# Performance work log

Measured on AMD Instinct MI355X. Metric: run time of the kernel, lower is better.

Reference implementation:

```python
import jax, jax.numpy as jnp
import numpy as np
import math

_B, _L, _D, _H = 4, 2048, 512, 8
_DH = _D // _H


def setup_inputs() -> dict:
    key = jax.random.key(0)
    ks = jax.random.split(key, 16)
    w_scale = 1.0 / math.sqrt(_D)
    def lin(kw, kb):
        W = jax.random.uniform(kw, (_D, _D), jnp.float32, -w_scale, w_scale)
        b = jax.random.uniform(kb, (_D,), jnp.float32, -w_scale, w_scale)
        return W, b
    Wq_w, Wq_b = lin(ks[0], ks[1])
    Wk_w, Wk_b = lin(ks[2], ks[3])
    Wv_w, Wv_b = lin(ks[4], ks[5])
    fc_w, fc_b = lin(ks[6], ks[7])
    Q = jax.random.normal(ks[8], (_B, _L, _D), jnp.float32)
    K = jax.random.normal(ks[9], (_B, _L, _D), jnp.float32)
    V = jax.random.normal(ks[10], (_B, _L, _D), jnp.float32)
    # E = torch.rand(L, DH): uniform [0,1), non-trainable buffer
    E = jax.random.uniform(ks[11], (_L, _DH), jnp.float32)
    # causal mask: True (1) where attention is disallowed -> gets -1e9
    mask = jnp.triu(jnp.ones((_L, _L), dtype=bool), k=1)[None, None]  # (1,1,L,L)
    return {"Q": Q, "K": K, "V": V, "mask": mask,
            "Wq_w": Wq_w, "Wq_b": Wq_b, "Wk_w": Wk_w, "Wk_b": Wk_b,
            "Wv_w": Wv_w, "Wv_b": Wv_b, "fc_w": fc_w, "fc_b": fc_b,
            "E": E, "H": _H}


def reference(Q, K, V, mask, Wq_w, Wq_b, Wk_w, Wk_b, Wv_w, Wv_b, fc_w, fc_b, E, H):
    B, Lq, D = Q.shape
    DH = D // H

    def proj(x, W, b):  # torch Linear: x @ W.T + b, then split heads -> (B,H,L,DH)
        y = x @ W.T + b
        return y.reshape(B, -1, H, DH).transpose(0, 2, 1, 3)

    q = proj(Q, Wq_w, Wq_b)
    k = proj(K, Wk_w, Wk_b)
    v = proj(V, Wv_w, Wv_b)
    Lk = k.shape[2]

    # _get_left_embedding: last Lq rows of E
    Eu = E[max(0, E.shape[0] - Lq):, :]            # (e, DH), e == Lq here
    e = Eu.shape[0]

    QE = jnp.einsum('bhld,ed->bhle', q, Eu)        # (B,H,Lq,e)
    # _qe_masking: keep QE[..., i, j] where j >= e-1-i (upper anti-triangle)
    i = jnp.arange(Lq)[:, None]
    j = jnp.arange(e)[None, :]
    keep = (i + j >= e - 1).astype(QE.dtype)
    QE = QE * keep

    # _skewing: pad one zero column, reshape, drop first row
    padded = jnp.pad(QE, ((0, 0), (0, 0), (0, 0), (1, 0)))   # (B,H,Lq,e+1)
    Srel = padded.reshape(B, H, e + 1, Lq)[:, :, 1:, :]      # (B,H,e,Lq)
    if Lk < Lq:
        Srel = Srel[:, :, :, :Lk]

    logits = (jnp.einsum('bhld,bhmd->bhlm', q, k) + Srel) / math.sqrt(DH)
    logits = logits + mask.astype(jnp.float32) * (-1e9)
    AW = jax.nn.softmax(logits, axis=-1)
    out = jnp.einsum('bhlm,bhmd->bhld', AW, v)               # (B,H,Lq,DH)
    out = out.transpose(0, 2, 1, 3).reshape(B, -1, D)        # (B,Lq,D)
    return out @ fc_w.T + fc_b
```

## Files before the change

kernel.cpp:

```cpp
#include <hip/hip_runtime.h>
#include <stdint.h>

typedef __bf16 bf16;
typedef float f32x4 __attribute__((ext_vector_type(4)));
typedef bf16 bf16x8 __attribute__((ext_vector_type(8)));
typedef bf16 bf16x4 __attribute__((ext_vector_type(4)));

#define MFMA16(a, b, c) __builtin_amdgcn_mfma_f32_16x16x32_bf16((a), (b), (c), 0, 0, 0)
#define EXP2F(x) __builtin_amdgcn_exp2f(x)

__device__ __forceinline__ void gll16(const void* g, void* l) {
  __builtin_amdgcn_global_load_lds((const __attribute__((address_space(1))) void*)g,
                                   (__attribute__((address_space(3))) void*)l, 16, 0, 0);
}

__global__ __launch_bounds__(256) void convert_all(
    const float4* __restrict__ Q, const float4* __restrict__ K, const float4* __restrict__ V,
    const float4* __restrict__ Wq, const float4* __restrict__ Wk, const float4* __restrict__ Wv,
    const float4* __restrict__ fcw, const float4* __restrict__ E,
    bf16x4* __restrict__ Xq, bf16x4* __restrict__ Xk, bf16x4* __restrict__ Xv,
    bf16x4* __restrict__ Wqb, bf16x4* __restrict__ Wkb, bf16x4* __restrict__ Wvb,
    bf16x4* __restrict__ fcb, bf16x4* __restrict__ Eb) {
  int i = blockIdx.x * 256 + threadIdx.x;
  const float4* s;
  bf16x4* d;
  int off;
  if (i < 1048576) { s = Q; d = Xq; off = i; }
  else if (i < 2097152) { s = K; d = Xk; off = i - 1048576; }
  else if (i < 3145728) { s = V; d = Xv; off = i - 2097152; }
  else if (i < 3211264) { s = Wq; d = Wqb; off = i - 3145728; }
  else if (i < 3276800) { s = Wk; d = Wkb; off = i - 3211264; }
  else if (i < 3342336) { s = Wv; d = Wvb; off = i - 3276800; }
  else if (i < 3407872) { s = fcw; d = fcb; off = i - 3342336; }
  else { s = E; d = Eb; off = i - 3407872; }
  float4 v = s[off];
  bf16x4 o;
  o[0] = (bf16)v.x; o[1] = (bf16)v.y; o[2] = (bf16)v.z; o[3] = (bf16)v.w;
  d[off] = o;
}

__device__ __forceinline__ void gemm_core(const bf16* __restrict__ A, const bf16* __restrict__ Bt,
                                          bf16* ldsA, bf16* ldsB, int m0, int n0,
                                          f32x4 acc[4][4]) {
  const int t = threadIdx.x;
  const int lane = t & 63, w = t >> 6;
  const int l15 = lane & 15, quad = lane >> 4;
  const int wm = w >> 1, wn = w & 1;
#pragma unroll
  for (int i = 0; i < 4; i++)
#pragma unroll
    for (int j = 0; j < 4; j++) acc[i][j] = (f32x4){0.f, 0.f, 0.f, 0.f};

  const int ch0 = t, ch1 = t + 256;
  const int r0 = ch0 >> 2, c0 = (ch0 & 3) ^ (r0 & 3);
  const int r1 = ch1 >> 2, c1 = (ch1 & 3) ^ (r1 & 3);

  int aoff[4], boff[4];
#pragma unroll
  for (int mt = 0; mt < 4; mt++) {
    int m = wm * 64 + mt * 16 + l15;
    aoff[mt] = (m << 6) + ((quad ^ (l15 & 3)) << 4);
    int n = wn * 64 + mt * 16 + l15;
    boff[mt] = (n << 6) + ((quad ^ (l15 & 3)) << 4);
  }
  bf16* ldsA1 = ldsA + w * 512;
  bf16* ldsA2 = ldsA + 2048 + w * 512;
  bf16* ldsB1 = ldsB + w * 512;
  bf16* ldsB2 = ldsB + 2048 + w * 512;

  for (int kt = 0; kt < 512; kt += 32) {
    gll16(A + (size_t)(m0 + r0) * 512 + kt + c0 * 8, ldsA1);
    gll16(A + (size_t)(m0 + r1) * 512 + kt + c1 * 8, ldsA2);
    gll16(Bt + (size_t)(n0 + r0) * 512 + kt + c0 * 8, ldsB1);
    gll16(Bt + (size_t)(n0 + r1) * 512 + kt + c1 * 8, ldsB2);
    __syncthreads();
    bf16x8 af[4], bfr[4];
#pragma unroll
    for (int mt = 0; mt < 4; mt++) af[mt] = *(const bf16x8*)((const char*)ldsA + aoff[mt]);
#pragma unroll
    for (int nt = 0; nt < 4; nt++) bfr[nt] = *(const bf16x8*)((const char*)ldsB + boff[nt]);
#pragma unroll
    for (int mt = 0; mt < 4; mt++)
#pragma unroll
      for (int nt = 0; nt < 4; nt++)
        acc[mt][nt] = MFMA16(af[mt], bfr[nt], acc[mt][nt]);
    __syncthreads();
  }
}

__global__ __launch_bounds__(256) void proj_gemm(
    const bf16* __restrict__ Xq, const bf16* __restrict__ Xk, const bf16* __restrict__ Xv,
    const bf16* __restrict__ Wq, const bf16* __restrict__ Wk, const bf16* __restrict__ Wv,
    const float* __restrict__ bq, const float* __restrict__ bk, const float* __restrict__ bv,
    bf16* __restrict__ qb, bf16* __restrict__ kb, bf16* __restrict__ vb) {
  __shared__ bf16 ldsA[128 * 32];
  __shared__ bf16 ldsB[128 * 32];
  const int z = blockIdx.z;
  const bf16* A = z == 0 ? Xq : (z == 1 ? Xk : Xv);
  const bf16* W = z == 0 ? Wq : (z == 1 ? Wk : Wv);
  const float* bias = z == 0 ? bq : (z == 1 ? bk : bv);
  bf16* out = z == 0 ? qb : (z == 1 ? kb : vb);
  const int m0 = blockIdx.x * 128, n0 = blockIdx.y * 128;
  f32x4 acc[4][4];
  gemm_core(A, W, ldsA, ldsB, m0, n0, acc);

  const int t = threadIdx.x;
  const int lane = t & 63, w = t >> 6;
  const int l15 = lane & 15, quad = lane >> 4;
  const int wm = w >> 1, wn = w & 1;
#pragma unroll
  for (int mt = 0; mt < 4; mt++)
#pragma unroll
    for (int nt = 0; nt < 4; nt++)
#pragma unroll
      for (int r = 0; r < 4; r++) {
        int gm = m0 + wm * 64 + mt * 16 + quad * 4 + r;
        int gn = n0 + wn * 64 + nt * 16 + l15;
        float v = acc[mt][nt][r] + bias[gn];
        int b = gm >> 11, l = gm & 2047, h = gn >> 6, d = gn & 63;
        out[(((size_t)(b * 8 + h)) * 2048 + l) * 64 + d] = (bf16)v;
      }
}

__global__ __launch_bounds__(256) void final_gemm(const bf16* __restrict__ A,
                                                  const bf16* __restrict__ W,
                                                  const float* __restrict__ bias,
                                                  float* __restrict__ out) {
  __shared__ bf16 ldsA[128 * 32];
  __shared__ bf16 ldsB[128 * 32];
  const int m0 = blockIdx.x * 128, n0 = blockIdx.y * 128;
  f32x4 acc[4][4];
  gemm_core(A, W, ldsA, ldsB, m0, n0, acc);

  const int t = threadIdx.x;
  const int lane = t & 63, w = t >> 6;
  const int l15 = lane & 15, quad = lane >> 4;
  const int wm = w >> 1, wn = w & 1;
#pragma unroll
  for (int mt = 0; mt < 4; mt++)
#pragma unroll
    for (int nt = 0; nt < 4; nt++)
#pragma unroll
      for (int r = 0; r < 4; r++) {
        int gm = m0 + wm * 64 + mt * 16 + quad * 4 + r;
        int gn = n0 + wn * 64 + nt * 16 + l15;
        out[(size_t)gm * 512 + gn] = acc[mt][nt][r] + bias[gn];
      }
}

__global__ __launch_bounds__(256) void transpose_v(const bf16* __restrict__ vbuf,
                                                   bf16* __restrict__ vT) {
  __shared__ bf16 tile[64][72];
  const int bh = blockIdx.y, l0 = blockIdx.x * 64;
  const bf16* src = vbuf + ((size_t)bh * 2048 + l0) * 64;
  bf16* dst = vT + (size_t)bh * 64 * 2048 + l0;
  const int t = threadIdx.x;
#pragma unroll
  for (int p = 0; p < 2; p++) {
    int ch = t + p * 256;
    int r = ch >> 3, c8 = ch & 7;
    *(bf16x8*)&tile[r][c8 * 8] = *(const bf16x8*)&src[(size_t)r * 64 + c8 * 8];
  }
  __syncthreads();
#pragma unroll
  for (int p = 0; p < 2; p++) {
    int ch = t + p * 256;
    int dr = ch >> 3, lc = ch & 7;
    bf16x8 v;
#pragma unroll
    for (int j = 0; j < 8; j++) v[j] = tile[lc * 8 + j][dr];
    *(bf16x8*)&dst[(size_t)dr * 2048 + lc * 8] = v;
  }
}

__global__ __launch_bounds__(256, 4) void attn_kernel(const bf16* __restrict__ qbuf,
                                                      const bf16* __restrict__ kbuf,
                                                      const bf16* __restrict__ vT,
                                                      const bf16* __restrict__ Eb,
                                                      bf16* __restrict__ attn) {
  __shared__ bf16 Kl[64 * 64];
  __shared__ bf16 Vl[64 * 64];
  __shared__ bf16 Pl[4][16 * 72];
  const int t = threadIdx.x, w = t >> 6, lane = t & 63;
  const int l15 = lane & 15, quad = lane >> 4;
  const int x = blockIdx.x;
  const int pid = x & 511, phase = x >> 9;
  const int a = pid & 15, bh = pid >> 4;
  const int t4 = phase ? a : 31 - a;
  const int i0 = t4 * 64 + w * 16;
  bf16* Pw = Pl[w];
  const bf16* qh = qbuf + (size_t)bh * 2048 * 64;
  const bf16* kh = kbuf + (size_t)bh * 2048 * 64;
  const bf16* vh = vT + (size_t)bh * 64 * 2048;

  const int sr0 = t >> 3, sc0 = (t & 7) ^ (sr0 & 7);
  const int sr1 = sr0 + 32;
  const int wb0 = (t & 192) * 8;
  const int wb1 = 2048 + wb0;

  int bpaddr[4];
  bool loA[4];
#pragma unroll
  for (int r = 0; r < 4; r++) {
    int u = quad * 4 + r;
    bpaddr[r] = (((l15 + 15 - u) & 15) + 16 * quad) * 4;
    loA[r] = (l15 <= u);
  }

  bf16x8 aq0, aq1;
  {
    const bf16* qrow = qh + (size_t)(i0 + l15) * 64 + quad * 8;
    aq0 = *(const bf16x8*)qrow;
    aq1 = *(const bf16x8*)(qrow + 32);
  }
  bf16x8 ones;
#pragma unroll
  for (int j = 0; j < 8; j++) ones[j] = (bf16)1.0f;

  f32x4 O[4], Osum;
  Osum = (f32x4){0.f, 0.f, 0.f, 0.f};
#pragma unroll
  for (int i = 0; i < 4; i++) O[i] = (f32x4){0.f, 0.f, 0.f, 0.f};
  const float sc = 0.125f * 1.44269504088896f;

  for (int jt = 0; jt <= t4; jt++) {
    const int j0 = jt * 64;
    const bool diag = (jt == t4);
    __syncthreads();
    gll16(kh + (size_t)(j0 + sr0) * 64 + sc0 * 8, (char*)Kl + wb0 * 2);
    gll16(kh + (size_t)(j0 + sr1) * 64 + sc0 * 8, (char*)Kl + wb1 * 2);
    gll16(vh + (size_t)sr0 * 2048 + j0 + sc0 * 8, (char*)Vl + wb0 * 2);
    gll16(vh + (size_t)sr1 * 2048 + j0 + sc0 * 8, (char*)Vl + wb1 * 2);
    const int ebase = 2047 - i0 + j0 - 15;
    f32x4 z[5];
#pragma unroll
    for (int nt = 0; nt < 5; nt++) {
      int er = ebase + nt * 16 + l15;
      er = er > 2047 ? 2047 : er;
      const bf16* erow = Eb + (size_t)er * 64 + quad * 8;
      bf16x8 b0 = *(const bf16x8*)erow;
      bf16x8 b1 = *(const bf16x8*)(erow + 32);
      f32x4 zz = (f32x4){0.f, 0.f, 0.f, 0.f};
      zz = MFMA16(aq0, b0, zz);
      z[nt] = MFMA16(aq1, b1, zz);
    }
    float Bp[5][4];
#pragma unroll
    for (int tn = 0; tn < 5; tn++)
#pragma unroll
      for (int r = 0; r < 4; r++)
        Bp[tn][r] = __int_as_float(
            __builtin_amdgcn_ds_bpermute(bpaddr[r], __float_as_int(z[tn][r])));
    __syncthreads();
    f32x4 s[4];
#pragma unroll
    for (int nt = 0; nt < 4; nt++) {
      int row = nt * 16 + l15;
      bf16x8 b0 = *(const bf16x8*)(Kl + ((row << 3) + (quad ^ (row & 7))) * 8);
      bf16x8 b1 = *(const bf16x8*)(Kl + ((row << 3) + ((quad + 4) ^ (row & 7))) * 8);
      f32x4 zz = (f32x4){0.f, 0.f, 0.f, 0.f};
      zz = MFMA16(aq0, b0, zz);
      s[nt] = MFMA16(aq1, b1, zz);
    }
    if (diag) {
#pragma unroll
      for (int nt = 0; nt < 4; nt++)
#pragma unroll
        for (int r = 0; r < 4; r++) {
          int u = quad * 4 + r;
          int j = nt * 16 + l15;
          float skew = loA[r] ? Bp[nt][r] : Bp[nt + 1][r];
          float logit = (s[nt][r] + skew) * sc;
          if (j0 + j > i0 + u) logit = -1e30f;
          Pw[u * 72 + j] = (bf16)EXP2F(logit);
        }
    } else {
#pragma unroll
      for (int nt = 0; nt < 4; nt++)
#pragma unroll
        for (int r = 0; r < 4; r++) {
          int u = quad * 4 + r;
          int j = nt * 16 + l15;
          float skew = loA[r] ? Bp[nt][r] : Bp[nt + 1][r];
          Pw[u * 72 + j] = (bf16)EXP2F((s[nt][r] + skew) * sc);
        }
    }
    bf16x8 pa0 = *(const bf16x8*)&Pw[l15 * 72 + quad * 8];
    bf16x8 pa1 = *(const bf16x8*)&Pw[l15 * 72 + 32 + quad * 8];
    Osum = MFMA16(pa0, ones, Osum);
    Osum = MFMA16(pa1, ones, Osum);
#pragma unroll
    for (int nt = 0; nt < 4; nt++) {
      int row = nt * 16 + l15;
      bf16x8 b0 = *(const bf16x8*)(Vl + ((row << 3) + (quad ^ (row & 7))) * 8);
      bf16x8 b1 = *(const bf16x8*)(Vl + ((row << 3) + ((quad + 4) ^ (row & 7))) * 8);
      O[nt] = MFMA16(pa0, b0, O[nt]);
      O[nt] = MFMA16(pa1, b1, O[nt]);
    }
  }
  const int b = bh >> 3, hh = bh & 7;
  float inv[4];
#pragma unroll
  for (int r = 0; r < 4; r++) inv[r] = 1.0f / Osum[r];
  bf16* orow = attn + ((size_t)(b * 2048 + i0)) * 512 + hh * 64;
#pragma unroll
  for (int nt = 0; nt < 4; nt++)
#pragma unroll
    for (int r = 0; r < 4; r++)
      orow[(size_t)(quad * 4 + r) * 512 + nt * 16 + l15] = (bf16)(O[nt][r] * inv[r]);
}

extern "C" void kernel_launch(void* const* d_in, const int* in_sizes, int n_in,
                              void* d_out, int out_size, void* d_ws, size_t ws_size,
                              hipStream_t stream) {
  const float* Q = (const float*)d_in[0];
  const float* K = (const float*)d_in[1];
  const float* V = (const float*)d_in[2];
  const float* Wq = (const float*)d_in[4];
  const float* bq = (const float*)d_in[5];
  const float* Wk = (const float*)d_in[6];
  const float* bk = (const float*)d_in[7];
  const float* Wv = (const float*)d_in[8];
  const float* bv = (const float*)d_in[9];
  const float* fcw = (const float*)d_in[10];
  const float* fcb = (const float*)d_in[11];
  const float* E = (const float*)d_in[12];

  char* ws = (char*)d_ws;
  bf16* Xq = (bf16*)(ws + 0);
  bf16* Xk = (bf16*)(ws + 8388608);
  bf16* Xv = (bf16*)(ws + 16777216);
  bf16* Wqb = (bf16*)(ws + 25165824);
  bf16* Wkb = (bf16*)(ws + 25690112);
  bf16* Wvb = (bf16*)(ws + 26214400);
  bf16* fcwb = (bf16*)(ws + 26738688);
  bf16* Eb = (bf16*)(ws + 27262976);
  bf16* qbuf = (bf16*)(ws + 27525120);
  bf16* kbuf = (bf16*)(ws + 35913728);
  bf16* vbuf = (bf16*)(ws + 44302336);
  bf16* vTb = Xk;
  bf16* attnb = Xq;

  convert_all<<<13440, 256, 0, stream>>>(
      (const float4*)Q, (const float4*)K, (const float4*)V, (const float4*)Wq,
      (const float4*)Wk, (const float4*)Wv, (const float4*)fcw, (const float4*)E,
      (bf16x4*)Xq, (bf16x4*)Xk, (bf16x4*)Xv, (bf16x4*)Wqb, (bf16x4*)Wkb,
      (bf16x4*)Wvb, (bf16x4*)fcwb, (bf16x4*)Eb);

  proj_gemm<<<dim3(64, 4, 3), 256, 0, stream>>>(Xq, Xk, Xv, Wqb, Wkb, Wvb, bq, bk, bv,
                                                qbuf, kbuf, vbuf);

  transpose_v<<<dim3(32, 32), 256, 0, stream>>>(vbuf, vTb);

  attn_kernel<<<1024, 256, 0, stream>>>(qbuf, kbuf, vTb, Eb, attnb);

  final_gemm<<<dim3(64, 4, 1), 256, 0, stream>>>(attnb, fcwb, fcb, (float*)d_out);
}
```

Baseline: 268.8 us.

## Double-buffer K/V tiles in LDS and carry skew E tile across iterations

The attention kernel now keeps two LDS buffers for the K and V tiles. It issues the global-to-LDS loads for the next key tile right after the barrier, so those loads overlap with the current tile's QK, softmax and PV work. The last relative-embedding skew tile of each iteration is kept in registers and reused as the first tile of the next, which removes one pair of E MFMAs and the matching bpermutes per iteration. In exchange, LDS use per block roughly doubles and the occupancy hint drops from 4 to 3 blocks per CU, so less latency can be hidden by other waves.

```diff
diff --git a/kernel.cpp b/kernel.cpp
--- a/kernel.cpp
+++ b/kernel.cpp
@@ -173,13 +173,13 @@
   }
 }
 
-__global__ __launch_bounds__(256, 4) void attn_kernel(const bf16* __restrict__ qbuf,
+__global__ __launch_bounds__(256, 3) void attn_kernel(const bf16* __restrict__ qbuf,
                                                       const bf16* __restrict__ kbuf,
                                                       const bf16* __restrict__ vT,
                                                       const bf16* __restrict__ Eb,
                                                       bf16* __restrict__ attn) {
-  __shared__ bf16 Kl[64 * 64];
-  __shared__ bf16 Vl[64 * 64];
+  __shared__ bf16 Kl[2][64 * 64];
+  __shared__ bf16 Vl[2][64 * 64];
   __shared__ bf16 Pl[4][16 * 72];
   const int t = threadIdx.x, w = t >> 6, lane = t & 63;
   const int l15 = lane & 15, quad = lane >> 4;
@@ -195,8 +195,8 @@
 
   const int sr0 = t >> 3, sc0 = (t & 7) ^ (sr0 & 7);
   const int sr1 = sr0 + 32;
-  const int wb0 = (t & 192) * 8;
-  const int wb1 = 2048 + wb0;
+  const int b0 = (t & 192) * 16;
+  const int b1 = 4096 + b0;
 
   int bpaddr[4];
   bool loA[4];
@@ -222,45 +222,73 @@
 #pragma unroll
   for (int i = 0; i < 4; i++) O[i] = (f32x4){0.f, 0.f, 0.f, 0.f};
   const float sc = 0.125f * 1.44269504088896f;
+  const int ebase0 = 2047 - i0 - 15;
+
+  gll16(kh + (size_t)sr0 * 64 + sc0 * 8, (char*)&Kl[0][0] + b0);
+  gll16(kh + (size_t)sr1 * 64 + sc0 * 8, (char*)&Kl[0][0] + b1);
+  gll16(vh + (size_t)sr0 * 2048 + sc0 * 8, (char*)&Vl[0][0] + b0);
+  gll16(vh + (size_t)sr1 * 2048 + sc0 * 8, (char*)&Vl[0][0] + b1);
+
+  float Bpc[4];
+  {
+    int er = ebase0 + l15;
+    er = er > 2047 ? 2047 : er;
+    const bf16* erow = Eb + (size_t)er * 64 + quad * 8;
+    bf16x8 e0 = *(const bf16x8*)erow;
+    bf16x8 e1 = *(const bf16x8*)(erow + 32);
+    f32x4 zz = (f32x4){0.f, 0.f, 0.f, 0.f};
+    zz = MFMA16(aq0, e0, zz);
+    zz = MFMA16(aq1, e1, zz);
+#pragma unroll
+    for (int r = 0; r < 4; r++)
+      Bpc[r] = __int_as_float(__builtin_amdgcn_ds_bpermute(bpaddr[r], __float_as_int(zz[r])));
+  }
 
   for (int jt = 0; jt <= t4; jt++) {
     const int j0 = jt * 64;
+    const int cur = jt & 1;
     const bool diag = (jt == t4);
-    __syncthreads();
-    gll16(kh + (size_t)(j0 + sr0) * 64 + sc0 * 8, (char*)Kl + wb0 * 2);
-    gll16(kh + (size_t)(j0 + sr1) * 64 + sc0 * 8, (char*)Kl + wb1 * 2);
-    gll16(vh + (size_t)sr0 * 2048 + j0 + sc0 * 8, (char*)Vl + wb0 * 2);
-    gll16(vh + (size_t)sr1 * 2048 + j0 + sc0 * 8, (char*)Vl + wb1 * 2);
-    const int ebase = 2047 - i0 + j0 - 15;
-    f32x4 z[5];
-#pragma unroll
-    for (int nt = 0; nt < 5; nt++) {
+    float Bp[5][4];
+#pragma unroll
+    for (int r = 0; r < 4; r++) Bp[0][r] = Bpc[r];
+    const int ebase = ebase0 + j0;
+#pragma unroll
+    for (int nt = 1; nt < 5; nt++) {
       int er = ebase + nt * 16 + l15;
       er = er > 2047 ? 2047 : er;
       const bf16* erow = Eb + (size_t)er * 64 + quad * 8;
-      bf16x8 b0 = *(const bf16x8*)erow;
-      bf16x8 b1 = *(const bf16x8*)(erow + 32);
+      bf16x8 e0 = *(const bf16x8*)erow;
+      bf16x8 e1 = *(const bf16x8*)(erow + 32);
       f32x4 zz = (f32x4){0.f, 0.f, 0.f, 0.f};
-      zz = MFMA16(aq0, b0, zz);
-      z[nt] = MFMA16(aq1, b1, zz);
-    }
-    float Bp[5][4];
-#pragma unroll
-    for (int tn = 0; tn < 5; tn++)
+      zz = MFMA16(aq0, e0, zz);
+      zz = MFMA16(aq1, e1, zz);
 #pragma unroll
       for (int r = 0; r < 4; r++)
-        Bp[tn][r] = __int_as_float(
-            __builtin_amdgcn_ds_bpermute(bpaddr[r], __float_as_int(z[tn][r])));
+        Bp[nt][r] =
+            __int_as_float(__builtin_amdgcn_ds_bpermute(bpaddr[r], __float_as_int(zz[r])));
+    }
+#pragma unroll
+    for (int r = 0; r < 4; r++) Bpc[r] = Bp[4][r];
+
     __syncthreads();
+    if (jt < t4) {
+      const int nb = cur ^ 1, nj = j0 + 64;
+      gll16(kh + (size_t)(nj + sr0) * 64 + sc0 * 8, (char*)&Kl[nb][0] + b0);
+      gll16(kh + (size_t)(nj + sr1) * 64 + sc0 * 8, (char*)&Kl[nb][0] + b1);
+      gll16(vh + (size_t)sr0 * 2048 + nj + sc0 * 8, (char*)&Vl[nb][0] + b0);
+      gll16(vh + (size_t)sr1 * 2048 + nj + sc0 * 8, (char*)&Vl[nb][0] + b1);
+    }
+    const bf16* Kc = Kl[cur];
+    const bf16* Vc = Vl[cur];
     f32x4 s[4];
 #pragma unroll
     for (int nt = 0; nt < 4; nt++) {
       int row = nt * 16 + l15;
-      bf16x8 b0 = *(const bf16x8*)(Kl + ((row << 3) + (quad ^ (row & 7))) * 8);
-      bf16x8 b1 = *(const bf16x8*)(Kl + ((row << 3) + ((quad + 4) ^ (row & 7))) * 8);
+      bf16x8 k0 = *(const bf16x8*)(Kc + ((row << 3) + (quad ^ (row & 7))) * 8);
+      bf16x8 k1 = *(const bf16x8*)(Kc + ((row << 3) + ((quad + 4) ^ (row & 7))) * 8);
       f32x4 zz = (f32x4){0.f, 0.f, 0.f, 0.f};
-      zz = MFMA16(aq0, b0, zz);
-      s[nt] = MFMA16(aq1, b1, zz);
+      zz = MFMA16(aq0, k0, zz);
+      s[nt] = MFMA16(aq1, k1, zz);
     }
     if (diag) {
 #pragma unroll
@@ -292,10 +320,10 @@
 #pragma unroll
     for (int nt = 0; nt < 4; nt++) {
       int row = nt * 16 + l15;
-      bf16x8 b0 = *(const bf16x8*)(Vl + ((row << 3) + (quad ^ (row & 7))) * 8);
-      bf16x8 b1 = *(const bf16x8*)(Vl + ((row << 3) + ((quad + 4) ^ (row & 7))) * 8);
-      O[nt] = MFMA16(pa0, b0, O[nt]);
-      O[nt] = MFMA16(pa1, b1, O[nt]);
+      bf16x8 v0 = *(const bf16x8*)(Vc + ((row << 3) + (quad ^ (row & 7))) * 8);
+      bf16x8 v1 = *(const bf16x8*)(Vc + ((row << 3) + ((quad + 4) ^ (row & 7))) * 8);
+      O[nt] = MFMA16(pa0, v0, O[nt]);
+      O[nt] = MFMA16(pa1, v1, O[nt]);
     }
   }
   const int b = bh >> 3, hh = bh & 7;
```

New measurement: 250.9 us. 1.07x faster.
